# Kernel optimization log

Hardware: AMD Instinct MI355X
Metric: run time of the kernel (lower is better)

The kernel has to match this reference:

```python
import jax, jax.numpy as jnp
import numpy as np

DIM = 1024
HEADS = 16
DIM_HEAD = 64
INNER = HEADS * DIM_HEAD
SCALE = DIM_HEAD ** -0.5
LN_EPS = 1e-5
MASK_VALUE = -np.finfo(np.float32).max


def setup_inputs() -> dict:
    key = jax.random.key(0)
    ks = jax.random.split(key, 3)
    x = jax.random.normal(ks[0], (2, 2048, DIM), dtype=jnp.float32)
    w_qkv = jax.random.normal(ks[1], (DIM, 3 * INNER), dtype=jnp.float32) * (DIM ** -0.5)
    w_out = jax.random.normal(ks[2], (INNER, DIM), dtype=jnp.float32) * (INNER ** -0.5)
    ln_gamma = jnp.ones((DIM,), dtype=jnp.float32)
    ln_beta = jnp.zeros((DIM,), dtype=jnp.float32)
    return {"x": x, "ln_gamma": ln_gamma, "ln_beta": ln_beta, "w_qkv": w_qkv, "w_out": w_out}


def reference(x, ln_gamma, ln_beta, w_qkv, w_out):
    b, n, _ = x.shape
    # LayerNorm
    mu = jnp.mean(x, axis=-1, keepdims=True)
    var = jnp.mean(jnp.square(x - mu), axis=-1, keepdims=True)
    xn = (x - mu) * jax.lax.rsqrt(var + LN_EPS) * ln_gamma + ln_beta
    # QKV projection, split into heads: b n (h d) -> b h n d
    qkv = xn @ w_qkv  # [b, n, 3*inner]
    q, k, v = jnp.split(qkv, 3, axis=-1)
    def to_heads(t):
        return t.reshape(b, n, HEADS, DIM_HEAD).transpose(0, 2, 1, 3)
    q, k, v = to_heads(q), to_heads(k), to_heads(v)
    # scaled scores with diagonal excluded
    dots = jnp.einsum('bhnd,bhmd->bhnm', q, k) * SCALE
    eye = jnp.eye(n, dtype=bool)
    dots = jnp.where(eye, MASK_VALUE, dots)
    attn = jax.nn.softmax(dots, axis=-1)
    out = jnp.einsum('bhnm,bhmd->bhnd', attn, v)
    out = out.transpose(0, 2, 1, 3).reshape(b, n, INNER)
    return out @ w_out
```

## Files before the change

### kernel.cpp

```cpp
#include <hip/hip_runtime.h>


#define DIMM   1024
#define NSEQ   2048
#define BATCH  2
#define HEADS  16
#define DHEAD  64
#define QKVN   3072
#define MROWS  4096

typedef float          f32x4  __attribute__((ext_vector_type(4)));
typedef __bf16         bf16x8 __attribute__((ext_vector_type(8)));
typedef __bf16         bf16x4 __attribute__((ext_vector_type(4)));
typedef unsigned short u16x8  __attribute__((ext_vector_type(8)));
typedef unsigned short u16x4  __attribute__((ext_vector_type(4)));

#define QSCALE (0.125f * 1.4426950408889634f)

#if __has_builtin(__builtin_amdgcn_exp2f)
#define EXP2(x) __builtin_amdgcn_exp2f(x)
#else
#define EXP2(x) exp2f(x)
#endif

__device__ __forceinline__ unsigned short f2bf(float f) {
  unsigned u = __builtin_bit_cast(unsigned, f);
  u += 0x7FFFu + ((u >> 16) & 1u);
  return (unsigned short)(u >> 16);
}
__device__ __forceinline__ bf16x8 as_bf(u16x8 v) { return __builtin_bit_cast(bf16x8, v); }

__device__ __forceinline__ u16x4 cvt4(f32x4 v) {
  bf16x4 b;
  b[0] = (__bf16)v[0]; b[1] = (__bf16)v[1]; b[2] = (__bf16)v[2]; b[3] = (__bf16)v[3];
  return __builtin_bit_cast(u16x4, b);
}

__device__ __forceinline__ void gl_lds16(const unsigned short* g, unsigned short* l) {
  __builtin_amdgcn_global_load_lds(
      (const __attribute__((address_space(1))) unsigned*)g,
      (__attribute__((address_space(3))) unsigned*)l, 16, 0, 0);
}

__device__ __forceinline__ bf16x8 lds_frag(const unsigned short* base, int row, int chunk) {
  return as_bf(*(const u16x8*)&base[row * 64 + ((chunk ^ (row & 7)) << 3)]);
}

__device__ __forceinline__ void transpose_tile(
    const float* __restrict__ src, unsigned short* __restrict__ dst,
    int R, int C, int bx, int by, int tid) {
  __shared__ float t[32][33];
  const int rb = by * 32, cb = bx * 32;
  const int r0 = tid >> 5;
  const int c  = tid & 31;
#pragma unroll
  for (int i = 0; i < 4; ++i)
    t[r0 + i * 8][c] = src[(rb + r0 + i * 8) * C + cb + c];
  __syncthreads();
#pragma unroll
  for (int i = 0; i < 4; ++i)
    dst[(cb + r0 + i * 8) * R + rb + c] = f2bf(t[c][r0 + i * 8]);
}

__global__ __launch_bounds__(256) void transpose2_kernel(
    const float* __restrict__ w_qkv, const float* __restrict__ w_out,
    unsigned short* __restrict__ wqkvT, unsigned short* __restrict__ woutT) {
  const int bx = blockIdx.x;
  if (bx < QKVN / 32) transpose_tile(w_qkv, wqkvT, DIMM, QKVN, bx, blockIdx.y, threadIdx.x);
  else                transpose_tile(w_out, woutT, DIMM, DIMM, bx - QKVN / 32, blockIdx.y, threadIdx.x);
}

__global__ __launch_bounds__(256) void ln_kernel(
    const float* __restrict__ x, const float* __restrict__ g,
    const float* __restrict__ be, unsigned short* __restrict__ xn) {
  const int row = blockIdx.x, tid = threadIdx.x;
  const int wave = tid >> 6, lane = tid & 63;
  const float4 v = *(const float4*)&x[row * DIMM + tid * 4];
  float s  = v.x + v.y + v.z + v.w;
  float s2 = v.x * v.x + v.y * v.y + v.z * v.z + v.w * v.w;
#pragma unroll
  for (int o = 32; o >= 1; o >>= 1) { s += __shfl_xor(s, o); s2 += __shfl_xor(s2, o); }
  __shared__ float ps[4], ps2[4];
  if (lane == 0) { ps[wave] = s; ps2[wave] = s2; }
  __syncthreads();
  s  = ps[0] + ps[1] + ps[2] + ps[3];
  s2 = ps2[0] + ps2[1] + ps2[2] + ps2[3];
  const float mu  = s * (1.0f / DIMM);
  const float var = s2 * (1.0f / DIMM) - mu * mu;
  const float rs  = rsqrtf(var + 1e-5f);
  const float4 gg = *(const float4*)&g[tid * 4];
  const float4 bb = *(const float4*)&be[tid * 4];
  u16x4 o;
  o[0] = f2bf((v.x - mu) * rs * gg.x + bb.x);
  o[1] = f2bf((v.y - mu) * rs * gg.y + bb.y);
  o[2] = f2bf((v.z - mu) * rs * gg.z + bb.z);
  o[3] = f2bf((v.w - mu) * rs * gg.w + bb.w);
  *(u16x4*)&xn[row * DIMM + tid * 4] = o;
}

template<bool SWAP>
__device__ __forceinline__ void gemm_core128(
    const unsigned short* __restrict__ A, const unsigned short* __restrict__ Bt,
    unsigned short* As, unsigned short* Bs, int bm, int bn, int tid,
    f32x4 (&acc)[4][4]) {
  const int wave = tid >> 6, lane = tid & 63;
  const int l15 = lane & 15, quad = lane >> 4;
  const int wm = wave >> 1, wn = wave & 1;
  const int lrow = lane >> 3;
  const int gcol = ((lane & 7) ^ lrow) << 3;
  const unsigned short* Ab = A  + (bm * 128 + wave * 32 + lrow) * DIMM + gcol;
  const unsigned short* Bb = Bt + (bn * 128 + wave * 32 + lrow) * DIMM + gcol;

  for (int k0 = 0; k0 < DIMM; k0 += 64) {
#pragma unroll
    for (int j = 0; j < 4; ++j) {
      gl_lds16(Ab + j * 8 * DIMM + k0, &As[(wave * 32 + j * 8) * 64]);
      gl_lds16(Bb + j * 8 * DIMM + k0, &Bs[(wave * 32 + j * 8) * 64]);
    }
    __syncthreads();
#pragma unroll
    for (int kk = 0; kk < 2; ++kk) {
      bf16x8 af[4], bfr[4];
#pragma unroll
      for (int mi = 0; mi < 4; ++mi) af[mi]  = lds_frag(As, wm * 64 + mi * 16 + l15, kk * 4 + quad);
#pragma unroll
      for (int ni = 0; ni < 4; ++ni) bfr[ni] = lds_frag(Bs, wn * 64 + ni * 16 + l15, kk * 4 + quad);
#pragma unroll
      for (int mi = 0; mi < 4; ++mi)
#pragma unroll
        for (int ni = 0; ni < 4; ++ni)
          acc[mi][ni] = SWAP
            ? __builtin_amdgcn_mfma_f32_16x16x32_bf16(bfr[ni], af[mi], acc[mi][ni], 0, 0, 0)
            : __builtin_amdgcn_mfma_f32_16x16x32_bf16(af[mi], bfr[ni], acc[mi][ni], 0, 0, 0);
    }
    __syncthreads();
  }
}

__global__ __launch_bounds__(256, 2) void gemm_qkv_kernel(
    const unsigned short* __restrict__ A, const unsigned short* __restrict__ Bt,
    unsigned short* __restrict__ qb, unsigned short* __restrict__ kb,
    unsigned short* __restrict__ vtb) {
  __shared__ __attribute__((aligned(16))) unsigned short As[128 * 64];
  __shared__ __attribute__((aligned(16))) unsigned short Bs[128 * 64];
  const int tid = threadIdx.x;
  const int bm = blockIdx.y, bn = blockIdx.x;
  const int lane = tid & 63, wave = tid >> 6;
  const int l15 = lane & 15, quad = lane >> 4;
  const int wm = wave >> 1, wn = wave & 1;
  f32x4 acc[4][4] = {};

  if (bn < 16) {
    gemm_core128<true>(A, Bt, As, Bs, bm, bn, tid, acc);
    const int colbase = bn * 128 + wn * 64;
    const int which = colbase >> 10;
    unsigned short* dst = which ? kb : qb;
    const float sc = which ? 1.0f : QSCALE;
#pragma unroll
    for (int mi = 0; mi < 4; ++mi) {
      const int m = bm * 128 + wm * 64 + mi * 16 + l15;
      const int bh0 = (m >> 11) * HEADS;
      const int n = m & 2047;
#pragma unroll
      for (int ni = 0; ni < 4; ++ni) {
        const int wc = (colbase & 1023) + ni * 16 + quad * 4;
        const int h = wc >> 6, dd = wc & 63;
        f32x4 v = acc[mi][ni] * sc;
        *(u16x4*)&dst[((bh0 + h) * NSEQ + n) * DHEAD + dd] = cvt4(v);
      }
    }
  } else {
    gemm_core128<false>(A, Bt, As, Bs, bm, bn, tid, acc);
    const int colbase = bn * 128 + wn * 64 - 2048;
#pragma unroll
    for (int mi = 0; mi < 4; ++mi) {
      const int m0 = bm * 128 + wm * 64 + mi * 16 + quad * 4;
      const int bh0 = (m0 >> 11) * HEADS;
      const int n0 = m0 & 2047;
#pragma unroll
      for (int ni = 0; ni < 4; ++ni) {
        const int vcol = colbase + ni * 16 + l15;
        const int h = vcol >> 6, dd = vcol & 63;
        *(u16x4*)&vtb[((bh0 + h) * DHEAD + dd) * NSEQ + n0] = cvt4(acc[mi][ni]);
      }
    }
  }
}

__global__ __launch_bounds__(256, 2) void attn_kernel(
    const unsigned short* __restrict__ qb, const unsigned short* __restrict__ kb,
    const unsigned short* __restrict__ vtb, unsigned short* __restrict__ attn_out) {
  __shared__ __attribute__((aligned(16))) unsigned short Ks[2][64 * 64];
  __shared__ __attribute__((aligned(16))) unsigned short Vts[2][64 * 64];
  __shared__ __attribute__((aligned(16))) unsigned short Ps[4][2][16][72];
  const int tid = threadIdx.x, wave = tid >> 6, lane = tid & 63;
  const int l15 = lane & 15, quad = lane >> 4;
  const int bh = blockIdx.x, qt = blockIdx.y;
  const int b = bh >> 4, h = bh & 15;
  const int qbase = qt * 128 + wave * 32;

  bf16x8 aq[2][2];
#pragma unroll
  for (int sub = 0; sub < 2; ++sub) {
    const unsigned short* qrow = qb + (bh * NSEQ + qbase + sub * 16 + l15) * DHEAD;
    aq[sub][0] = as_bf(*(const u16x8*)(qrow + quad * 8));
    aq[sub][1] = as_bf(*(const u16x8*)(qrow + 32 + quad * 8));
  }

  float lsum[2] = {0.f, 0.f};
  f32x4 occ[2][4] = {};

  const int lrow = lane >> 3;
  const int gcol = ((lane & 7) ^ lrow) << 3;
  const unsigned short* Kb = kb  + (bh * NSEQ + wave * 16 + lrow) * DHEAD + gcol;
  const unsigned short* Vb = vtb + (bh * DHEAD + wave * 16 + lrow) * NSEQ + gcol;

  gl_lds16(Kb,             &Ks[0][(wave * 16) * 64]);
  gl_lds16(Kb + 8 * DHEAD, &Ks[0][(wave * 16 + 8) * 64]);
  gl_lds16(Vb,             &Vts[0][(wave * 16) * 64]);
  gl_lds16(Vb + 8 * NSEQ,  &Vts[0][(wave * 16 + 8) * 64]);

  const int diag_it = qt * 2 + (wave >> 1);

  for (int it = 0; it < NSEQ / 64; ++it) {
    const int cur = it & 1;
    __syncthreads();
    if (it < NSEQ / 64 - 1) {
      const unsigned short* Kn = Kb + (it + 1) * 64 * DHEAD;
      const unsigned short* Vn = Vb + (it + 1) * 64;
      gl_lds16(Kn,             &Ks[cur ^ 1][(wave * 16) * 64]);
      gl_lds16(Kn + 8 * DHEAD, &Ks[cur ^ 1][(wave * 16 + 8) * 64]);
      gl_lds16(Vn,             &Vts[cur ^ 1][(wave * 16) * 64]);
      gl_lds16(Vn + 8 * NSEQ,  &Vts[cur ^ 1][(wave * 16 + 8) * 64]);
    }
    bf16x8 ak[2][4], av[2][4];
#pragma unroll
    for (int kk = 0; kk < 2; ++kk)
#pragma unroll
      for (int ct = 0; ct < 4; ++ct) {
        ak[kk][ct] = lds_frag(&Ks[cur][0],  ct * 16 + l15, kk * 4 + quad);
        av[kk][ct] = lds_frag(&Vts[cur][0], ct * 16 + l15, kk * 4 + quad);
      }
#pragma unroll
    for (int sub = 0; sub < 2; ++sub) {
      f32x4 scc[4];
#pragma unroll
      for (int ct = 0; ct < 4; ++ct) scc[ct] = (f32x4){-32.f, -32.f, -32.f, -32.f};
#pragma unroll
      for (int kk = 0; kk < 2; ++kk)
#pragma unroll
        for (int ct = 0; ct < 4; ++ct)
          scc[ct] = __builtin_amdgcn_mfma_f32_16x16x32_bf16(ak[kk][ct], aq[sub][kk], scc[ct], 0, 0, 0);
#pragma unroll
      for (int ct = 0; ct < 4; ++ct)
#pragma unroll
        for (int r = 0; r < 4; ++r) scc[ct][r] = EXP2(scc[ct][r]);

      if (it == diag_it) {
        const int kvo_want = (wave & 1) * 32 + sub * 16 + l15;
#pragma unroll
        for (int ct = 0; ct < 4; ++ct)
#pragma unroll
          for (int r = 0; r < 4; ++r)
            if (ct * 16 + quad * 4 + r == kvo_want) scc[ct][r] = 0.f;
      }

      f32x4 ps4 = (scc[0] + scc[1]) + (scc[2] + scc[3]);
      lsum[sub] += (ps4[0] + ps4[1]) + (ps4[2] + ps4[3]);

#pragma unroll
      for (int ct = 0; ct < 4; ++ct)
        *(u16x4*)&Ps[wave][sub][l15][ct * 16 + quad * 4] = cvt4(scc[ct]);

#pragma unroll
      for (int kk = 0; kk < 2; ++kk) {
        bf16x8 bp = as_bf(*(const u16x8*)&Ps[wave][sub][l15][kk * 32 + quad * 8]);
#pragma unroll
        for (int ct = 0; ct < 4; ++ct)
          occ[sub][ct] = __builtin_amdgcn_mfma_f32_16x16x32_bf16(av[kk][ct], bp, occ[sub][ct], 0, 0, 0);
      }
    }
  }
#pragma unroll
  for (int sub = 0; sub < 2; ++sub) {
    float l = lsum[sub];
    l += __shfl_xor(l, 16);
    l += __shfl_xor(l, 32);
    const float rl = __builtin_amdgcn_rcpf(l);
    const int qg = qbase + sub * 16 + l15;
#pragma unroll
    for (int ct = 0; ct < 4; ++ct) {
      f32x4 ov = occ[sub][ct] * rl;
      *(u16x4*)&attn_out[(b * NSEQ + qg) * DIMM + h * DHEAD + ct * 16 + quad * 4] = cvt4(ov);
    }
  }
}

__global__ __launch_bounds__(256, 2) void gemm_out_kernel(
    const unsigned short* __restrict__ A,
    const unsigned short* __restrict__ Bt,
    float* __restrict__ out) {
  __shared__ __attribute__((aligned(16))) unsigned short As[128 * 64];
  __shared__ __attribute__((aligned(16))) unsigned short Bs[128 * 64];
  const int tid = threadIdx.x;
  const int bm = blockIdx.y, bn = blockIdx.x;
  f32x4 acc[4][4] = {};
  gemm_core128<true>(A, Bt, As, Bs, bm, bn, tid, acc);

  const int lane = tid & 63, wave = tid >> 6;
  const int l15 = lane & 15, quad = lane >> 4;
  const int wm = wave >> 1, wn = wave & 1;
#pragma unroll
  for (int mi = 0; mi < 4; ++mi) {
    const int m = bm * 128 + wm * 64 + mi * 16 + l15;
#pragma unroll
    for (int ni = 0; ni < 4; ++ni) {
      const int col = bn * 128 + wn * 64 + ni * 16 + quad * 4;
      *(f32x4*)&out[m * DIMM + col] = acc[mi][ni];
    }
  }
}

extern "C" void kernel_launch(void* const* d_in, const int* in_sizes, int n_in,
                              void* d_out, int out_size, void* d_ws, size_t ws_size,
                              hipStream_t stream) {
  const float* x     = (const float*)d_in[0];
  const float* gamma = (const float*)d_in[1];
  const float* beta  = (const float*)d_in[2];
  const float* w_qkv = (const float*)d_in[3];
  const float* w_out = (const float*)d_in[4];
  float* out = (float*)d_out;

  char* ws = (char*)d_ws;
  unsigned short* xn    = (unsigned short*)(ws);
  unsigned short* wqkvT = (unsigned short*)(ws + 8388608);
  unsigned short* woutT = (unsigned short*)(ws + 14680064);
  unsigned short* qbuf  = (unsigned short*)(ws + 16777216);
  unsigned short* kbuf  = (unsigned short*)(ws + 25165824);
  unsigned short* vtbuf = (unsigned short*)(ws + 33554432);
  unsigned short* attnb = (unsigned short*)(ws + 41943040);

  transpose2_kernel<<<dim3((QKVN + DIMM) / 32, DIMM / 32), 256, 0, stream>>>(w_qkv, w_out, wqkvT, woutT);
  ln_kernel<<<MROWS, 256, 0, stream>>>(x, gamma, beta, xn);
  gemm_qkv_kernel<<<dim3(24, MROWS / 128), 256, 0, stream>>>(xn, wqkvT, qbuf, kbuf, vtbuf);
  attn_kernel<<<dim3(BATCH * HEADS, NSEQ / 128), 256, 0, stream>>>(qbuf, kbuf, vtbuf, attnb);
  gemm_out_kernel<<<dim3(DIMM / 128, MROWS / 128), 256, 0, stream>>>(attnb, woutT, out);
}
```

Measured before the change: 189.3 us.

## Double-buffer GEMM LDS tiles, merge LN and transpose, shrink out-GEMM M tile

Both GEMM kernels now keep two LDS buffers and prefetch the next K slice while the MFMAs run on the current one, leaving one barrier per iteration instead of two. The layernorm and weight-transpose kernels are merged into one launch to save a kernel launch. The output GEMM uses 64-row M tiles, doubling its grid to 512 blocks for better CU occupancy. The cost is doubled LDS per block, which may cut residency, and a runtime swap branch inside the QKV inner loop.

```diff
diff --git a/kernel.cpp b/kernel.cpp
--- a/kernel.cpp
+++ b/kernel.cpp
@@ -62,96 +62,106 @@
     dst[(cb + r0 + i * 8) * R + rb + c] = f2bf(t[c][r0 + i * 8]);
 }
 
-__global__ __launch_bounds__(256) void transpose2_kernel(
-    const float* __restrict__ w_qkv, const float* __restrict__ w_out,
+__global__ __launch_bounds__(256) void prep_kernel(
+    const float* __restrict__ x, const float* __restrict__ g,
+    const float* __restrict__ be, const float* __restrict__ w_qkv,
+    const float* __restrict__ w_out, unsigned short* __restrict__ xn,
     unsigned short* __restrict__ wqkvT, unsigned short* __restrict__ woutT) {
-  const int bx = blockIdx.x;
-  if (bx < QKVN / 32) transpose_tile(w_qkv, wqkvT, DIMM, QKVN, bx, blockIdx.y, threadIdx.x);
-  else                transpose_tile(w_out, woutT, DIMM, DIMM, bx - QKVN / 32, blockIdx.y, threadIdx.x);
-}
-
-__global__ __launch_bounds__(256) void ln_kernel(
-    const float* __restrict__ x, const float* __restrict__ g,
-    const float* __restrict__ be, unsigned short* __restrict__ xn) {
-  const int row = blockIdx.x, tid = threadIdx.x;
-  const int wave = tid >> 6, lane = tid & 63;
-  const float4 v = *(const float4*)&x[row * DIMM + tid * 4];
-  float s  = v.x + v.y + v.z + v.w;
-  float s2 = v.x * v.x + v.y * v.y + v.z * v.z + v.w * v.w;
-#pragma unroll
-  for (int o = 32; o >= 1; o >>= 1) { s += __shfl_xor(s, o); s2 += __shfl_xor(s2, o); }
-  __shared__ float ps[4], ps2[4];
-  if (lane == 0) { ps[wave] = s; ps2[wave] = s2; }
-  __syncthreads();
-  s  = ps[0] + ps[1] + ps[2] + ps[3];
-  s2 = ps2[0] + ps2[1] + ps2[2] + ps2[3];
-  const float mu  = s * (1.0f / DIMM);
-  const float var = s2 * (1.0f / DIMM) - mu * mu;
-  const float rs  = rsqrtf(var + 1e-5f);
-  const float4 gg = *(const float4*)&g[tid * 4];
-  const float4 bb = *(const float4*)&be[tid * 4];
-  u16x4 o;
-  o[0] = f2bf((v.x - mu) * rs * gg.x + bb.x);
-  o[1] = f2bf((v.y - mu) * rs * gg.y + bb.y);
-  o[2] = f2bf((v.z - mu) * rs * gg.z + bb.z);
-  o[3] = f2bf((v.w - mu) * rs * gg.w + bb.w);
-  *(u16x4*)&xn[row * DIMM + tid * 4] = o;
-}
-
-template<bool SWAP>
-__device__ __forceinline__ void gemm_core128(
+  const int bid = blockIdx.x, tid = threadIdx.x;
+  if (bid < MROWS) {
+    const int row = bid;
+    const int wave = tid >> 6, lane = tid & 63;
+    const float4 v = *(const float4*)&x[row * DIMM + tid * 4];
+    float s  = v.x + v.y + v.z + v.w;
+    float s2 = v.x * v.x + v.y * v.y + v.z * v.z + v.w * v.w;
+#pragma unroll
+    for (int o = 32; o >= 1; o >>= 1) { s += __shfl_xor(s, o); s2 += __shfl_xor(s2, o); }
+    __shared__ float ps[4], ps2[4];
+    if (lane == 0) { ps[wave] = s; ps2[wave] = s2; }
+    __syncthreads();
+    s  = ps[0] + ps[1] + ps[2] + ps[3];
+    s2 = ps2[0] + ps2[1] + ps2[2] + ps2[3];
+    const float mu  = s * (1.0f / DIMM);
+    const float var = s2 * (1.0f / DIMM) - mu * mu;
+    const float rs  = rsqrtf(var + 1e-5f);
+    const float4 gg = *(const float4*)&g[tid * 4];
+    const float4 bb = *(const float4*)&be[tid * 4];
+    u16x4 o;
+    o[0] = f2bf((v.x - mu) * rs * gg.x + bb.x);
+    o[1] = f2bf((v.y - mu) * rs * gg.y + bb.y);
+    o[2] = f2bf((v.z - mu) * rs * gg.z + bb.z);
+    o[3] = f2bf((v.w - mu) * rs * gg.w + bb.w);
+    *(u16x4*)&xn[row * DIMM + tid * 4] = o;
+  } else {
+    const int t = bid - MROWS;
+    const int bx = t & 127, by = t >> 7;
+    if (bx < QKVN / 32) transpose_tile(w_qkv, wqkvT, DIMM, QKVN, bx, by, tid);
+    else                transpose_tile(w_out, woutT, DIMM, DIMM, bx - QKVN / 32, by, tid);
+  }
+}
+
+__global__ __launch_bounds__(256, 2) void gemm_qkv_kernel(
     const unsigned short* __restrict__ A, const unsigned short* __restrict__ Bt,
-    unsigned short* As, unsigned short* Bs, int bm, int bn, int tid,
-    f32x4 (&acc)[4][4]) {
-  const int wave = tid >> 6, lane = tid & 63;
+    unsigned short* __restrict__ qb, unsigned short* __restrict__ kb,
+    unsigned short* __restrict__ vtb) {
+  __shared__ __attribute__((aligned(16))) unsigned short As[2 * 128 * 64];
+  __shared__ __attribute__((aligned(16))) unsigned short Bs[2 * 128 * 64];
+  const int tid = threadIdx.x;
+  const int bm = blockIdx.y, bn = blockIdx.x;
+  const int lane = tid & 63, wave = tid >> 6;
   const int l15 = lane & 15, quad = lane >> 4;
   const int wm = wave >> 1, wn = wave & 1;
   const int lrow = lane >> 3;
   const int gcol = ((lane & 7) ^ lrow) << 3;
   const unsigned short* Ab = A  + (bm * 128 + wave * 32 + lrow) * DIMM + gcol;
   const unsigned short* Bb = Bt + (bn * 128 + wave * 32 + lrow) * DIMM + gcol;
-
-  for (int k0 = 0; k0 < DIMM; k0 += 64) {
-#pragma unroll
-    for (int j = 0; j < 4; ++j) {
-      gl_lds16(Ab + j * 8 * DIMM + k0, &As[(wave * 32 + j * 8) * 64]);
-      gl_lds16(Bb + j * 8 * DIMM + k0, &Bs[(wave * 32 + j * 8) * 64]);
-    }
+  const bool swap = (bn < 16);
+  f32x4 acc[4][4] = {};
+
+#pragma unroll
+  for (int j = 0; j < 4; ++j) {
+    gl_lds16(Ab + j * 8 * DIMM, &As[(wave * 32 + j * 8) * 64]);
+    gl_lds16(Bb + j * 8 * DIMM, &Bs[(wave * 32 + j * 8) * 64]);
+  }
+  for (int it = 0; it < DIMM / 64; ++it) {
+    const int cur = it & 1;
     __syncthreads();
+    if (it < DIMM / 64 - 1) {
+      const int k0 = (it + 1) * 64;
+      unsigned short* An = &As[(cur ^ 1) * 8192];
+      unsigned short* Bn = &Bs[(cur ^ 1) * 8192];
+#pragma unroll
+      for (int j = 0; j < 4; ++j) {
+        gl_lds16(Ab + j * 8 * DIMM + k0, &An[(wave * 32 + j * 8) * 64]);
+        gl_lds16(Bb + j * 8 * DIMM + k0, &Bn[(wave * 32 + j * 8) * 64]);
+      }
+    }
+    const unsigned short* Ac = &As[cur * 8192];
+    const unsigned short* Bc = &Bs[cur * 8192];
 #pragma unroll
     for (int kk = 0; kk < 2; ++kk) {
       bf16x8 af[4], bfr[4];
 #pragma unroll
-      for (int mi = 0; mi < 4; ++mi) af[mi]  = lds_frag(As, wm * 64 + mi * 16 + l15, kk * 4 + quad);
-#pragma unroll
-      for (int ni = 0; ni < 4; ++ni) bfr[ni] = lds_frag(Bs, wn * 64 + ni * 16 + l15, kk * 4 + quad);
-#pragma unroll
-      for (int mi = 0; mi < 4; ++mi)
-#pragma unroll
-        for (int ni = 0; ni < 4; ++ni)
-          acc[mi][ni] = SWAP
-            ? __builtin_amdgcn_mfma_f32_16x16x32_bf16(bfr[ni], af[mi], acc[mi][ni], 0, 0, 0)
-            : __builtin_amdgcn_mfma_f32_16x16x32_bf16(af[mi], bfr[ni], acc[mi][ni], 0, 0, 0);
-    }
-    __syncthreads();
-  }
-}
-
-__global__ __launch_bounds__(256, 2) void gemm_qkv_kernel(
-    const unsigned short* __restrict__ A, const unsigned short* __restrict__ Bt,
-    unsigned short* __restrict__ qb, unsigned short* __restrict__ kb,
-    unsigned short* __restrict__ vtb) {
-  __shared__ __attribute__((aligned(16))) unsigned short As[128 * 64];
-  __shared__ __attribute__((aligned(16))) unsigned short Bs[128 * 64];
-  const int tid = threadIdx.x;
-  const int bm = blockIdx.y, bn = blockIdx.x;
-  const int lane = tid & 63, wave = tid >> 6;
-  const int l15 = lane & 15, quad = lane >> 4;
-  const int wm = wave >> 1, wn = wave & 1;
-  f32x4 acc[4][4] = {};
-
-  if (bn < 16) {
-    gemm_core128<true>(A, Bt, As, Bs, bm, bn, tid, acc);
+      for (int mi = 0; mi < 4; ++mi) af[mi]  = lds_frag(Ac, wm * 64 + mi * 16 + l15, kk * 4 + quad);
+#pragma unroll
+      for (int ni = 0; ni < 4; ++ni) bfr[ni] = lds_frag(Bc, wn * 64 + ni * 16 + l15, kk * 4 + quad);
+      if (swap) {
+#pragma unroll
+        for (int mi = 0; mi < 4; ++mi)
+#pragma unroll
+          for (int ni = 0; ni < 4; ++ni)
+            acc[mi][ni] = __builtin_amdgcn_mfma_f32_16x16x32_bf16(bfr[ni], af[mi], acc[mi][ni], 0, 0, 0);
+      } else {
+#pragma unroll
+        for (int mi = 0; mi < 4; ++mi)
+#pragma unroll
+          for (int ni = 0; ni < 4; ++ni)
+            acc[mi][ni] = __builtin_amdgcn_mfma_f32_16x16x32_bf16(af[mi], bfr[ni], acc[mi][ni], 0, 0, 0);
+      }
+    }
+  }
+
+  if (swap) {
     const int colbase = bn * 128 + wn * 64;
     const int which = colbase >> 10;
     unsigned short* dst = which ? kb : qb;
@@ -170,7 +180,6 @@
       }
     }
   } else {
-    gemm_core128<false>(A, Bt, As, Bs, bm, bn, tid, acc);
     const int colbase = bn * 128 + wn * 64 - 2048;
 #pragma unroll
     for (int mi = 0; mi < 4; ++mi) {
@@ -300,19 +309,55 @@
     const unsigned short* __restrict__ A,
     const unsigned short* __restrict__ Bt,
     float* __restrict__ out) {
-  __shared__ __attribute__((aligned(16))) unsigned short As[128 * 64];
-  __shared__ __attribute__((aligned(16))) unsigned short Bs[128 * 64];
+  __shared__ __attribute__((aligned(16))) unsigned short As[2 * 64 * 64];
+  __shared__ __attribute__((aligned(16))) unsigned short Bs[2 * 128 * 64];
   const int tid = threadIdx.x;
   const int bm = blockIdx.y, bn = blockIdx.x;
-  f32x4 acc[4][4] = {};
-  gemm_core128<true>(A, Bt, As, Bs, bm, bn, tid, acc);
-
   const int lane = tid & 63, wave = tid >> 6;
   const int l15 = lane & 15, quad = lane >> 4;
   const int wm = wave >> 1, wn = wave & 1;
-#pragma unroll
-  for (int mi = 0; mi < 4; ++mi) {
-    const int m = bm * 128 + wm * 64 + mi * 16 + l15;
+  const int lrow = lane >> 3;
+  const int gcol = ((lane & 7) ^ lrow) << 3;
+  const unsigned short* Ab = A  + (bm * 64 + wave * 16 + lrow) * DIMM + gcol;
+  const unsigned short* Bb = Bt + (bn * 128 + wave * 32 + lrow) * DIMM + gcol;
+  f32x4 acc[2][4] = {};
+
+#pragma unroll
+  for (int j = 0; j < 2; ++j) gl_lds16(Ab + j * 8 * DIMM, &As[(wave * 16 + j * 8) * 64]);
+#pragma unroll
+  for (int j = 0; j < 4; ++j) gl_lds16(Bb + j * 8 * DIMM, &Bs[(wave * 32 + j * 8) * 64]);
+
+  for (int it = 0; it < DIMM / 64; ++it) {
+    const int cur = it & 1;
+    __syncthreads();
+    if (it < DIMM / 64 - 1) {
+      const int k0 = (it + 1) * 64;
+      unsigned short* An = &As[(cur ^ 1) * 4096];
+      unsigned short* Bn = &Bs[(cur ^ 1) * 8192];
+#pragma unroll
+      for (int j = 0; j < 2; ++j) gl_lds16(Ab + j * 8 * DIMM + k0, &An[(wave * 16 + j * 8) * 64]);
+#pragma unroll
+      for (int j = 0; j < 4; ++j) gl_lds16(Bb + j * 8 * DIMM + k0, &Bn[(wave * 32 + j * 8) * 64]);
+    }
+    const unsigned short* Ac = &As[cur * 4096];
+    const unsigned short* Bc = &Bs[cur * 8192];
+#pragma unroll
+    for (int kk = 0; kk < 2; ++kk) {
+      bf16x8 af[2], bfr[4];
+#pragma unroll
+      for (int mi = 0; mi < 2; ++mi) af[mi]  = lds_frag(Ac, wm * 32 + mi * 16 + l15, kk * 4 + quad);
+#pragma unroll
+      for (int ni = 0; ni < 4; ++ni) bfr[ni] = lds_frag(Bc, wn * 64 + ni * 16 + l15, kk * 4 + quad);
+#pragma unroll
+      for (int mi = 0; mi < 2; ++mi)
+#pragma unroll
+        for (int ni = 0; ni < 4; ++ni)
+          acc[mi][ni] = __builtin_amdgcn_mfma_f32_16x16x32_bf16(bfr[ni], af[mi], acc[mi][ni], 0, 0, 0);
+    }
+  }
+#pragma unroll
+  for (int mi = 0; mi < 2; ++mi) {
+    const int m = bm * 64 + wm * 32 + mi * 16 + l15;
 #pragma unroll
     for (int ni = 0; ni < 4; ++ni) {
       const int col = bn * 128 + wn * 64 + ni * 16 + quad * 4;
@@ -340,9 +385,9 @@
   unsigned short* vtbuf = (unsigned short*)(ws + 33554432);
   unsigned short* attnb = (unsigned short*)(ws + 41943040);
 
-  transpose2_kernel<<<dim3((QKVN + DIMM) / 32, DIMM / 32), 256, 0, stream>>>(w_qkv, w_out, wqkvT, woutT);
-  ln_kernel<<<MROWS, 256, 0, stream>>>(x, gamma, beta, xn);
+  prep_kernel<<<MROWS + (QKVN + DIMM) / 32 * (DIMM / 32), 256, 0, stream>>>(
+      x, gamma, beta, w_qkv, w_out, xn, wqkvT, woutT);
   gemm_qkv_kernel<<<dim3(24, MROWS / 128), 256, 0, stream>>>(xn, wqkvT, qbuf, kbuf, vtbuf);
   attn_kernel<<<dim3(BATCH * HEADS, NSEQ / 128), 256, 0, stream>>>(qbuf, kbuf, vtbuf, attnb);
-  gemm_out_kernel<<<dim3(DIMM / 128, MROWS / 128), 256, 0, stream>>>(attnb, woutT, out);
-}
+  gemm_out_kernel<<<dim3(DIMM / 128, MROWS / 64), 256, 0, stream>>>(attnb, woutT, out);
+}
```

Result: no change. 188.1 us (-0.6%).
